# Kernel tuning notes

Measured on AMD Instinct MI355X. Metric: run time of the kernel, lower is better.

Reference implementation:

```python
import jax, jax.numpy as jnp
import numpy as np

N, E, G = 50000, 200000, 2000        # nodes, directed edges, graphs in batch
F_IN, HID, HEADS = 64, 128, 4
DM = HID * HEADS                      # 512, concat GAT output dim
EPS = 1e-5
NEG_SLOPE = 0.2                       # PyG GATConv LeakyReLU slope


def setup_inputs() -> dict:
    key = jax.random.key(0)
    ks = jax.random.split(key, 40)
    rn = lambda k, s, sc: jax.random.normal(k, s, jnp.float32) * sc
    inp = {}
    inp["x"] = rn(ks[0], (N, F_IN), 1.0)
    inp["edge_index"] = jax.random.randint(ks[1], (2, E), 0, N)
    inp["batch"] = jnp.sort(jax.random.randint(ks[2], (N,), 0, G))
    dims = [F_IN, DM, DM]
    for l in range(3):
        d = dims[l]
        inp["W%d" % l] = rn(ks[3 + 4 * l], (d, DM), 1.0 / np.sqrt(d))
        inp["as%d" % l] = rn(ks[4 + 4 * l], (HEADS, HID), 0.1)
        inp["ad%d" % l] = rn(ks[5 + 4 * l], (HEADS, HID), 0.1)
        inp["b%d" % l] = jnp.zeros((DM,), jnp.float32)
        inp["g%d" % l] = jnp.ones((DM,), jnp.float32)
        inp["be%d" % l] = jnp.zeros((DM,), jnp.float32)
    inp["c1w"] = rn(ks[20], (2 * DM, HID), 1.0 / np.sqrt(2 * DM))
    inp["c1b"] = jnp.zeros((HID,), jnp.float32)
    inp["c2w"] = rn(ks[21], (HID, HID // 2), 1.0 / np.sqrt(HID))
    inp["c2b"] = jnp.zeros((HID // 2,), jnp.float32)
    inp["c3w"] = rn(ks[22], (HID // 2, 1), 1.0 / np.sqrt(HID // 2))
    inp["c3b"] = jnp.zeros((1,), jnp.float32)
    return inp


def _gat(x, src, dst, W, a_s, a_d, b):
    """PyG GATConv (heads=HEADS, concat) with self-loops already in src/dst."""
    n = x.shape[0]
    h = (x @ W).reshape(n, HEADS, HID)                     # [N,H,D]
    s_src = jnp.sum(h * a_s, -1)                           # [N,H]
    s_dst = jnp.sum(h * a_d, -1)                           # [N,H]
    e = jax.nn.leaky_relu(s_src[src] + s_dst[dst], NEG_SLOPE)  # [Et,H]
    # segment softmax over incoming edges of each dst node (stable)
    m = jax.lax.stop_gradient(jax.ops.segment_max(e, dst, num_segments=n))
    ex = jnp.exp(e - m[dst])
    alpha = ex / jax.ops.segment_sum(ex, dst, num_segments=n)[dst]
    out = jax.ops.segment_sum(h[src] * alpha[:, :, None], dst, num_segments=n)
    return out.reshape(n, HEADS * HID) + b


def _bn(x, g, b):
    mu = jnp.mean(x, 0)
    var = jnp.var(x, 0)
    return (x - mu) * jax.lax.rsqrt(var + EPS) * g + b


def _forward(x, edge_index, batch, layers, c1w, c1b, c2w, c2b, c3w, c3b):
    loops = jnp.arange(N)
    src = jnp.concatenate([edge_index[0], loops])          # add self-loops
    dst = jnp.concatenate([edge_index[1], loops])
    for (W, a_s, a_d, b, g, be) in layers:
        x = jax.nn.relu(_bn(_gat(x, src, dst, W, a_s, a_d, b), g, be))
    cnt = jax.ops.segment_sum(jnp.ones((N,), x.dtype), batch, num_segments=G)
    mean = jax.ops.segment_sum(x, batch, num_segments=G) / jnp.maximum(cnt, 1.0)[:, None]
    mx = jax.ops.segment_max(x, batch, num_segments=G)
    mx = jnp.where(cnt[:, None] > 0, mx, 0.0)
    h = jnp.concatenate([mean, mx], 1)                     # [G, 2*DM]
    h = jax.nn.relu(h @ c1w + c1b)
    h = jax.nn.relu(h @ c2w + c2b)
    return jax.nn.sigmoid(h @ c3w + c3b).squeeze(-1)       # [G]


def reference(x, edge_index, batch, W0, as0, ad0, b0, g0, be0, W1, as1, ad1, b1, g1, be1, W2, as2, ad2, b2, g2, be2, c1w, c1b, c2w, c2b, c3w, c3b):
    layers = [(W0, as0, ad0, b0, g0, be0), (W1, as1, ad1, b1, g1, be1), (W2, as2, ad2, b2, g2, be2)]
    return _forward(x, edge_index, batch, layers, c1w, c1b, c2w, c2b, c3w, c3b)
```

## Files before the change

### kernel.cpp

```cpp
#include <hip/hip_runtime.h>

#define N_NODES 50000
#define E_EDGES 200000
#define ET_EDGES (E_EDGES + N_NODES)
#define G_GRAPHS 2000
#define F_IN 64
#define HID 128
#define HEADS 4
#define DM 512
#define BN_EPS 1e-5f
#define NEG_SLOPE 0.2f
#define YBLK 391
#define NCHUNK (YBLK / 8)

typedef unsigned short ushort_t;
typedef float floatx4 __attribute__((ext_vector_type(4)));
typedef short short8 __attribute__((ext_vector_type(8)));

__device__ __forceinline__ float b2f(unsigned int u) {
    union { unsigned int i; float f; } v; v.i = u << 16; return v.f;
}
__device__ __forceinline__ ushort_t f2b(float f) {
    union { float f; unsigned int i; } v; v.f = f;
    unsigned int r = v.i + 0x7FFFu + ((v.i >> 16) & 1u);
    return (ushort_t)(r >> 16);
}
__device__ __forceinline__ void unpack8(uint4 v, float* f) {
    f[0] = b2f(v.x & 0xffffu); f[1] = b2f(v.x >> 16);
    f[2] = b2f(v.y & 0xffffu); f[3] = b2f(v.y >> 16);
    f[4] = b2f(v.z & 0xffffu); f[5] = b2f(v.z >> 16);
    f[6] = b2f(v.w & 0xffffu); f[7] = b2f(v.w >> 16);
}
__device__ __forceinline__ void glds16(const ushort_t* g, ushort_t* l) {
    __builtin_amdgcn_global_load_lds(
        (const __attribute__((address_space(1))) unsigned int*)g,
        (__attribute__((address_space(3))) unsigned int*)l, 16, 0, 0);
}

#define XN (N_NODES * F_IN)
#define W0N (F_IN * DM)
#define W1N (DM * DM)
__global__ __launch_bounds__(256) void k_prep(const float* __restrict__ x,
                                              const float* __restrict__ w0,
                                              const float* __restrict__ w1,
                                              const float* __restrict__ w2,
                                              ushort_t* __restrict__ Xb,
                                              ushort_t* __restrict__ Wh0,
                                              ushort_t* __restrict__ Wh1,
                                              ushort_t* __restrict__ Wh2) {
    int t = blockIdx.x * 256 + threadIdx.x;
    if (t < XN) { Xb[t] = f2b(x[t]); return; }
    t -= XN;
    if (t < W0N) {
        int k = t >> 9, n = t & 511;
        Wh0[(size_t)n * F_IN + k] = f2b(w0[t]);
        return;
    }
    t -= W0N;
    if (t < W1N) {
        int k = t >> 9, n = t & 511;
        Wh1[(size_t)n * DM + k] = f2b(w1[t]);
        return;
    }
    t -= W1N;
    if (t < W1N) {
        int k = t >> 9, n = t & 511;
        Wh2[(size_t)n * DM + k] = f2b(w2[t]);
    }
}

__global__ __launch_bounds__(256) void k_wsprep(const float* __restrict__ w0,
                                                const float* __restrict__ as0, const float* __restrict__ ad0,
                                                const float* __restrict__ w1,
                                                const float* __restrict__ as1, const float* __restrict__ ad1,
                                                const float* __restrict__ w2,
                                                const float* __restrict__ as2, const float* __restrict__ ad2,
                                                ushort_t* __restrict__ ws0,
                                                ushort_t* __restrict__ ws1,
                                                ushort_t* __restrict__ ws2) {
    int b = blockIdx.x;
    int l = b >> 3, h = (b >> 1) & 3, v = b & 1;
    const float* w = l == 0 ? w0 : l == 1 ? w1 : w2;
    const float* a = v == 0 ? (l == 0 ? as0 : l == 1 ? as1 : as2)
                            : (l == 0 ? ad0 : l == 1 ? ad1 : ad2);
    ushort_t* o = l == 0 ? ws0 : l == 1 ? ws1 : ws2;
    int K = l == 0 ? F_IN : DM;
    __shared__ float av[HID];
    int t = threadIdx.x;
    if (t < HID) av[t] = a[h * HID + t];
    __syncthreads();
    for (int k = t; k < K; k += 256) {
        const float* wr = w + (size_t)k * DM + h * HID;
        float s = 0.f;
#pragma unroll 8
        for (int c = 0; c < HID; ++c) s += wr[c] * av[c];
        o[(h * 2 + v) * K + k] = f2b(s);
    }
}

__global__ __launch_bounds__(256) void k_mgemm(const ushort_t* __restrict__ A,
                                               const ushort_t* __restrict__ Bh,
                                               const ushort_t* __restrict__ ws,
                                               ushort_t* __restrict__ C,
                                               float* __restrict__ ssrc,
                                               float* __restrict__ sdst,
                                               int M, int K) {
    __shared__ __align__(16) ushort_t Ash[2][128 * 32];
    __shared__ __align__(16) ushort_t Bsh[2][128 * 32];
    int bid = blockIdx.x;
    int head, yb;
    if (bid < NCHUNK * 32) {
        int chunk = bid >> 5, pos = bid & 31;
        yb = chunk * 8 + (pos & 7);
        head = pos >> 3;
    } else {
        int rem = bid - NCHUNK * 32;
        head = rem & 3;
        yb = NCHUNK * 8 + (rem >> 2);
    }
    int m0 = yb * 128, n0 = head * 128;
    int tid = threadIdx.x;
    int lane = tid & 63, wave = tid >> 6;
    int wm = (wave >> 1) * 64, wn = (wave & 1) * 64;
    floatx4 acc[4][4] = {};
    floatx4 sacc[4] = {};
    int lrow = lane >> 2, lchunk = lane & 3;
    int fs = (lrow & 3) ^ ((lrow >> 2) & 3);
    int schunk = lchunk ^ fs;
    int ar0 = wave * 16 + lrow;
    int ar1 = ar0 + 64;
    int gr0 = m0 + ar0; if (gr0 >= M) gr0 = M - 1;
    int gr1 = m0 + ar1; if (gr1 >= M) gr1 = M - 1;
    const ushort_t* gA0 = A + (size_t)gr0 * K + schunk * 8;
    const ushort_t* gA1 = A + (size_t)gr1 * K + schunk * 8;
    const ushort_t* gB0 = Bh + (size_t)(n0 + ar0) * K + schunk * 8;
    const ushort_t* gB1 = Bh + (size_t)(n0 + ar1) * K + schunk * 8;
    int rF = lane & 15, q = lane >> 4;
    int swz = ((q ^ (rF & 3) ^ ((rF >> 2) & 3))) * 8;
    const ushort_t* wsp = ws + (size_t)(head * 2 + (rF & 1)) * K + q * 8;
    auto STAGE = [&](int b, int koff) {
        glds16(gA0 + koff, &Ash[b][(wave * 16) * 32]);
        glds16(gA1 + koff, &Ash[b][(wave * 16 + 64) * 32]);
        glds16(gB0 + koff, &Bsh[b][(wave * 16) * 32]);
        glds16(gB1 + koff, &Bsh[b][(wave * 16 + 64) * 32]);
    };
    STAGE(0, 0);
    __syncthreads();
    int cur = 0;
    for (int k0 = 0; k0 < K; k0 += 32) {
        if (k0 + 32 < K) STAGE(cur ^ 1, k0 + 32);
        short8 sf = *(const short8*)&wsp[k0];
        short8 af[4], bf[4];
#pragma unroll
        for (int i = 0; i < 4; ++i)
            af[i] = *(const short8*)&Ash[cur][(wm + i * 16 + rF) * 32 + swz];
#pragma unroll
        for (int j = 0; j < 4; ++j)
            bf[j] = *(const short8*)&Bsh[cur][(wn + j * 16 + rF) * 32 + swz];
#pragma unroll
        for (int i = 0; i < 4; ++i) {
            sacc[i] = __builtin_amdgcn_mfma_f32_16x16x32_bf16(af[i], sf, sacc[i], 0, 0, 0);
#pragma unroll
            for (int j = 0; j < 4; ++j)
                acc[i][j] = __builtin_amdgcn_mfma_f32_16x16x32_bf16(af[i], bf[j], acc[i][j], 0, 0, 0);
        }
        __syncthreads();
        cur ^= 1;
    }
    int cr = (lane >> 4) * 4, cc = lane & 15;
#pragma unroll
    for (int i = 0; i < 4; ++i) {
#pragma unroll
        for (int r = 0; r < 4; ++r) {
            int gr = m0 + wm + i * 16 + cr + r;
            if (gr < M) {
#pragma unroll
                for (int j = 0; j < 4; ++j)
                    C[(size_t)gr * DM + n0 + wn + j * 16 + cc] = f2b(acc[i][j][r]);
                if (cc == 0) ssrc[gr * 4 + head] = sacc[i][r];
                else if (cc == 1) sdst[gr * 4 + head] = sacc[i][r];
            }
        }
    }
}

__global__ __launch_bounds__(256) void k_bnapply(const ushort_t* __restrict__ X,
                                                 const float* __restrict__ stat,
                                                 const float* __restrict__ gam,
                                                 const float* __restrict__ bet,
                                                 ushort_t* __restrict__ Y) {
    __shared__ float sc[512], sh[512];
    int t = threadIdx.x;
    for (int f = t; f < 512; f += 256) {
        float mu = stat[f] * (1.f / (float)N_NODES);
        float var = fmaxf(stat[512 + f] * (1.f / (float)N_NODES) - mu * mu, 0.f);
        float rs = rsqrtf(var + BN_EPS);
        float s = gam[f] * rs;
        sc[f] = s;
        sh[f] = bet[f] - mu * s;
    }
    __syncthreads();
    int c8 = (t & 63) * 8;
    const float* scp = sc + c8;
    const float* shp = sh + c8;
    for (int n = blockIdx.x * 4 + (t >> 6); n < N_NODES; n += gridDim.x * 4) {
        uint4 v = *(const uint4*)&X[(size_t)n * DM + c8];
        float fv[8]; unpack8(v, fv);
        uint4 ov; unsigned* po = (unsigned*)&ov;
#pragma unroll
        for (int j = 0; j < 4; ++j) {
            unsigned lo = f2b(fmaxf(fv[2 * j] * scp[2 * j] + shp[2 * j], 0.f));
            unsigned hi = f2b(fmaxf(fv[2 * j + 1] * scp[2 * j + 1] + shp[2 * j + 1], 0.f));
            po[j] = lo | (hi << 16);
        }
        *(uint4*)&Y[(size_t)n * DM + c8] = ov;
    }
}

__global__ void k_degree(const int* __restrict__ ei, int* __restrict__ deg) {
    int e = blockIdx.x * blockDim.x + threadIdx.x;
    if (e >= ET_EDGES) return;
    int d = (e < E_EDGES) ? ei[E_EDGES + e] : (e - E_EDGES);
    atomicAdd(&deg[d], 1);
}

__global__ __launch_bounds__(1024) void k_scan3(const int* __restrict__ deg,
                                                int* __restrict__ offs,
                                                int* __restrict__ cursor) {
    __shared__ int wsum[16];
    __shared__ int carry;
    int t = threadIdx.x;
    int lane = t & 63, wv = t >> 6;
    if (t == 0) carry = 0;
    __syncthreads();
    for (int base = 0; base < N_NODES; base += 1024) {
        int i = base + t;
        int v = (i < N_NODES) ? deg[i] : 0;
        int x = v;
#pragma unroll
        for (int off = 1; off < 64; off <<= 1) {
            int y = __shfl_up(x, off);
            if (lane >= off) x += y;
        }
        if (lane == 63) wsum[wv] = x;
        __syncthreads();
        int wpre = 0;
#pragma unroll
        for (int w = 0; w < 16; ++w) wpre += (w < wv) ? wsum[w] : 0;
        int incl = wpre + x;
        if (i < N_NODES) { int o = carry + (incl - v); offs[i] = o; cursor[i] = o; }
        __syncthreads();
        if (t == 1023) carry += incl;
        __syncthreads();
    }
    if (t == 0) offs[N_NODES] = carry;
}

__global__ void k_scatter(const int* __restrict__ ei, int* __restrict__ cursor,
                          int* __restrict__ csr_src) {
    int e = blockIdx.x * blockDim.x + threadIdx.x;
    if (e >= ET_EDGES) return;
    int sv, d;
    if (e < E_EDGES) { sv = ei[e]; d = ei[E_EDGES + e]; } else { sv = d = e - E_EDGES; }
    int pos = atomicAdd(&cursor[d], 1);
    csr_src[pos] = sv;
}

__global__ void k_gbounds(const int* __restrict__ batch, int* __restrict__ gstart) {
    int i = blockIdx.x * blockDim.x + threadIdx.x;
    if (i >= N_NODES) return;
    int b = batch[i];
    int p = (i == 0) ? -1 : batch[i - 1];
    for (int g = p + 1; g <= b; ++g) gstart[g] = i;
    if (i == N_NODES - 1)
        for (int g = b + 1; g <= G_GRAPHS; ++g) gstart[g] = N_NODES;
}

__global__ __launch_bounds__(256) void k_aggregate(const ushort_t* __restrict__ H,
                                                   const float* __restrict__ ssrc,
                                                   const float* __restrict__ sdst,
                                                   const int* __restrict__ offs,
                                                   const int* __restrict__ csr_src,
                                                   const float* __restrict__ bias,
                                                   ushort_t* __restrict__ out) {
    int wave = threadIdx.x >> 6, lane = threadIdx.x & 63;
    int n = blockIdx.x * 4 + wave;
    if (n >= N_NODES) return;
    int beg = offs[n], end = offs[n + 1];
    int hl = lane >> 4, li = lane & 15;
    float sdh = sdst[n * 4 + hl];
    float m = -1e30f, s = 0.f;
    for (int e = beg + li; e < end; e += 16) {
        float sc = ssrc[csr_src[e] * 4 + hl] + sdh;
        sc = sc > 0.f ? sc : NEG_SLOPE * sc;
        if (sc > m) { s = s * __expf(m - sc) + 1.f; m = sc; }
        else s += __expf(sc - m);
    }
#pragma unroll
    for (int mk = 1; mk < 16; mk <<= 1) {
        float om = __shfl_xor(m, mk), os = __shfl_xor(s, mk);
        float mn = fmaxf(m, om);
        s = s * __expf(m - mn) + os * __expf(om - mn);
        m = mn;
    }
    float mh = m, inv = 1.f / s;
    float acc[8] = { 0.f, 0.f, 0.f, 0.f, 0.f, 0.f, 0.f, 0.f };
    int e = beg;
    for (; e + 4 <= end; e += 4) {
        int sv0 = csr_src[e], sv1 = csr_src[e + 1];
        int sv2 = csr_src[e + 2], sv3 = csr_src[e + 3];
        float s0 = ssrc[sv0 * 4 + hl], s1 = ssrc[sv1 * 4 + hl];
        float s2 = ssrc[sv2 * 4 + hl], s3 = ssrc[sv3 * 4 + hl];
        uint4 h0 = *(const uint4*)&H[(size_t)sv0 * DM + lane * 8];
        uint4 h1 = *(const uint4*)&H[(size_t)sv1 * DM + lane * 8];
        uint4 h2 = *(const uint4*)&H[(size_t)sv2 * DM + lane * 8];
        uint4 h3 = *(const uint4*)&H[(size_t)sv3 * DM + lane * 8];
        s0 += sdh; s0 = s0 > 0.f ? s0 : NEG_SLOPE * s0;
        s1 += sdh; s1 = s1 > 0.f ? s1 : NEG_SLOPE * s1;
        s2 += sdh; s2 = s2 > 0.f ? s2 : NEG_SLOPE * s2;
        s3 += sdh; s3 = s3 > 0.f ? s3 : NEG_SLOPE * s3;
        float a0 = __expf(s0 - mh) * inv, a1 = __expf(s1 - mh) * inv;
        float a2 = __expf(s2 - mh) * inv, a3 = __expf(s3 - mh) * inv;
        float f0[8], f1[8], f2[8], f3[8];
        unpack8(h0, f0); unpack8(h1, f1); unpack8(h2, f2); unpack8(h3, f3);
#pragma unroll
        for (int j = 0; j < 8; ++j)
            acc[j] += a0 * f0[j] + a1 * f1[j] + a2 * f2[j] + a3 * f3[j];
    }
    for (; e < end; ++e) {
        int sv = csr_src[e];
        float sc = ssrc[sv * 4 + hl] + sdh;
        sc = sc > 0.f ? sc : NEG_SLOPE * sc;
        float alpha = __expf(sc - mh) * inv;
        uint4 hv = *(const uint4*)&H[(size_t)sv * DM + lane * 8];
        float f[8]; unpack8(hv, f);
#pragma unroll
        for (int j = 0; j < 8; ++j) acc[j] += alpha * f[j];
    }
    const float* bp = bias + lane * 8;
    float4 b0 = *(const float4*)bp;
    float4 b1 = *(const float4*)(bp + 4);
    acc[0] += b0.x; acc[1] += b0.y; acc[2] += b0.z; acc[3] += b0.w;
    acc[4] += b1.x; acc[5] += b1.y; acc[6] += b1.z; acc[7] += b1.w;
    uint4 ov; unsigned* po = (unsigned*)&ov;
#pragma unroll
    for (int j = 0; j < 4; ++j)
        po[j] = (unsigned)f2b(acc[2 * j]) | ((unsigned)f2b(acc[2 * j + 1]) << 16);
    *(uint4*)&out[(size_t)n * DM + lane * 8] = ov;
}

#define BN_ROWS 125
__global__ __launch_bounds__(256) void k_bnstats(const ushort_t* __restrict__ X,
                                                 float* __restrict__ stat) {
    int t = threadIdx.x;
    int c2 = t * 2;
    int beg = blockIdx.x * BN_ROWS;
    int end = beg + BN_ROWS; if (end > N_NODES) end = N_NODES;
    float s0 = 0.f, s1 = 0.f, q0 = 0.f, q1 = 0.f;
    for (int n = beg; n < end; ++n) {
        unsigned v = *(const unsigned*)&X[(size_t)n * DM + c2];
        float x0 = b2f(v & 0xffffu), x1 = b2f(v >> 16);
        s0 += x0; s1 += x1;
        q0 += x0 * x0; q1 += x1 * x1;
    }
    atomicAdd(&stat[c2], s0);
    atomicAdd(&stat[c2 + 1], s1);
    atomicAdd(&stat[512 + c2], q0);
    atomicAdd(&stat[512 + c2 + 1], q1);
}

__global__ __launch_bounds__(64) void k_pool(const ushort_t* __restrict__ X,
                                             const int* __restrict__ gstart,
                                             const float* __restrict__ stat,
                                             const float* __restrict__ gam,
                                             const float* __restrict__ bet,
                                             float* __restrict__ pool) {
    int g = blockIdx.x, t = threadIdx.x;
    int beg = gstart[g], end = gstart[g + 1];
    float sc[8], sh[8];
#pragma unroll
    for (int j = 0; j < 8; ++j) {
        int f = t * 8 + j;
        float mu = stat[f] * (1.f / (float)N_NODES);
        float var = fmaxf(stat[512 + f] * (1.f / (float)N_NODES) - mu * mu, 0.f);
        float rs = rsqrtf(var + BN_EPS);
        sc[j] = gam[f] * rs;
        sh[j] = bet[f] - mu * sc[j];
    }
    float sum[8] = { 0 }, mx[8];
#pragma unroll
    for (int j = 0; j < 8; ++j) mx[j] = -1e30f;
    for (int nn = beg; nn < end; ++nn) {
        uint4 xv = *(const uint4*)&X[(size_t)nn * DM + t * 8];
        float f[8]; unpack8(xv, f);
#pragma unroll
        for (int j = 0; j < 8; ++j) {
            f[j] = fmaxf(f[j] * sc[j] + sh[j], 0.f);
            sum[j] += f[j]; mx[j] = fmaxf(mx[j], f[j]);
        }
    }
    float cnt = (float)(end - beg);
    float inv = cnt > 0.f ? 1.f / cnt : 0.f;
#pragma unroll
    for (int j = 0; j < 8; ++j) {
        pool[(size_t)g * 1024 + t * 8 + j] = sum[j] * inv;
        pool[(size_t)g * 1024 + 512 + t * 8 + j] = cnt > 0.f ? mx[j] : 0.f;
    }
}

__global__ __launch_bounds__(256) void k_mlp(const float* __restrict__ pool,
                                             const float* __restrict__ c1w,
                                             const float* __restrict__ c1b,
                                             const float* __restrict__ c2w,
                                             const float* __restrict__ c2b,
                                             const float* __restrict__ c3w,
                                             const float* __restrict__ c3b,
                                             float* __restrict__ out) {
    __shared__ float row[1024];
    __shared__ float part[128];
    __shared__ float h1[128];
    __shared__ float h2[64];
    int g = blockIdx.x, t = threadIdx.x;
    for (int i = t; i < 1024; i += 256) row[i] = pool[(size_t)g * 1024 + i];
    __syncthreads();
    int half = t >> 7, c = t & 127;
    int k0 = half * 512;
    float a1 = 0.f;
#pragma unroll 8
    for (int k = 0; k < 512; ++k) a1 += row[k0 + k] * c1w[(k0 + k) * 128 + c];
    if (half) part[c] = a1;
    __syncthreads();
    if (!half) h1[c] = fmaxf(a1 + part[c] + c1b[c], 0.f);
    __syncthreads();
    if (t < 64) {
        float a2 = c2b[t];
#pragma unroll 8
        for (int k = 0; k < 128; ++k) a2 += h1[k] * c2w[k * 64 + t];
        h2[t] = fmaxf(a2, 0.f);
    }
    __syncthreads();
    if (t < 64) {
        float p = h2[t] * c3w[t];
#pragma unroll
        for (int off = 32; off > 0; off >>= 1) p += __shfl_down(p, off);
        if (t == 0) {
            float z = p + c3b[0];
            out[g] = 1.f / (1.f + __expf(-z));
        }
    }
}

extern "C" void kernel_launch(void* const* d_in, const int* in_sizes, int n_in,
                              void* d_out, int out_size, void* d_ws, size_t ws_size,
                              hipStream_t stream) {
    const float* x = (const float*)d_in[0];
    const int* ei = (const int*)d_in[1];
    const int* batch = (const int*)d_in[2];
    const float* c1w = (const float*)d_in[21];
    const float* c1b = (const float*)d_in[22];
    const float* c2w = (const float*)d_in[23];
    const float* c2b = (const float*)d_in[24];
    const float* c3w = (const float*)d_in[25];
    const float* c3b = (const float*)d_in[26];

    char* p = (char*)d_ws;
    auto carve = [&](size_t bytes) -> char* {
        char* r = p; p += (bytes + 255) & ~(size_t)255; return r;
    };
    ushort_t* buf0   = (ushort_t*)carve((size_t)N_NODES * DM * 2);
    ushort_t* buf1   = (ushort_t*)carve((size_t)N_NODES * DM * 2);
    ushort_t* Xb     = (ushort_t*)carve((size_t)N_NODES * F_IN * 2);
    ushort_t* Wh0    = (ushort_t*)carve((size_t)F_IN * DM * 2);
    ushort_t* Wh1    = (ushort_t*)carve((size_t)DM * DM * 2);
    ushort_t* Wh2    = (ushort_t*)carve((size_t)DM * DM * 2);
    ushort_t* ws0    = (ushort_t*)carve((size_t)8 * F_IN * 2);
    ushort_t* ws1    = (ushort_t*)carve((size_t)8 * DM * 2);
    ushort_t* ws2    = (ushort_t*)carve((size_t)8 * DM * 2);
    float*    ssrc   = (float*)carve((size_t)N_NODES * 4 * 4);
    float*    sdst   = (float*)carve((size_t)N_NODES * 4 * 4);
    int*      deg    = (int*)carve((size_t)N_NODES * 4);
    int*      offs   = (int*)carve((size_t)(N_NODES + 1) * 4);
    int*      cursor = (int*)carve((size_t)N_NODES * 4);
    int*      csrsrc = (int*)carve((size_t)ET_EDGES * 4);
    float*    bnstat = (float*)carve(3 * 1024 * 4);
    int*      gstart = (int*)carve((size_t)(G_GRAPHS + 1) * 4);
    float*    pool   = (float*)carve((size_t)G_GRAPHS * 1024 * 4);

    hipMemsetAsync(deg, 0, (size_t)N_NODES * 4, stream);
    hipMemsetAsync(bnstat, 0, 3 * 1024 * 4, stream);
    k_degree<<<(ET_EDGES + 255) / 256, 256, 0, stream>>>(ei, deg);
    k_scan3<<<1, 1024, 0, stream>>>(deg, offs, cursor);
    k_scatter<<<(ET_EDGES + 255) / 256, 256, 0, stream>>>(ei, cursor, csrsrc);
    k_gbounds<<<(N_NODES + 255) / 256, 256, 0, stream>>>(batch, gstart);
    {
        int total = XN + W0N + 2 * W1N;
        k_prep<<<(total + 255) / 256, 256, 0, stream>>>(
            x, (const float*)d_in[3], (const float*)d_in[9], (const float*)d_in[15],
            Xb, Wh0, Wh1, Wh2);
    }
    k_wsprep<<<24, 256, 0, stream>>>(
        (const float*)d_in[3], (const float*)d_in[4], (const float*)d_in[5],
        (const float*)d_in[9], (const float*)d_in[10], (const float*)d_in[11],
        (const float*)d_in[15], (const float*)d_in[16], (const float*)d_in[17],
        ws0, ws1, ws2);

    const ushort_t* Whs[3] = { Wh0, Wh1, Wh2 };
    const ushort_t* wss[3] = { ws0, ws1, ws2 };
    const float* pgam = nullptr;
    const float* pbet = nullptr;
    const ushort_t* in = Xb;
    for (int l = 0; l < 3; ++l) {
        int K = (l == 0) ? F_IN : DM;
        const float* bia = (const float*)d_in[6 + 6 * l];
        const float* gam = (const float*)d_in[7 + 6 * l];
        const float* bet = (const float*)d_in[8 + 6 * l];
        ushort_t* h   = (l % 2 == 0) ? buf1 : buf0;
        ushort_t* agg = (l % 2 == 0) ? buf0 : buf1;

        k_mgemm<<<4 * YBLK, 256, 0, stream>>>(
            in, Whs[l], wss[l], h, ssrc, sdst, N_NODES, K);
        k_aggregate<<<(N_NODES + 3) / 4, 256, 0, stream>>>(h, ssrc, sdst, offs, csrsrc, bia, agg);
        k_bnstats<<<(N_NODES + BN_ROWS - 1) / BN_ROWS, 256, 0, stream>>>(agg, bnstat + l * 1024);
        if (l < 2)
            k_bnapply<<<2048, 256, 0, stream>>>(agg, bnstat + l * 1024, gam, bet, h);
        in = h;
        pgam = gam; pbet = bet;
    }
    k_pool<<<G_GRAPHS, 64, 0, stream>>>(buf0, gstart, bnstat + 2 * 1024, pgam, pbet, pool);
    k_mlp<<<G_GRAPHS, 256, 0, stream>>>(pool, c1w, c1b, c2w, c2b, c3w, c3b,
                                        (float*)d_out);
}
```

Before: 705.3 us.

## Triple-buffer GEMM tiles with vmcnt waits and stage score weights in LDS

The projection GEMM moves from a double-buffered loop with two full __syncthreads per iteration to a three-stage ring. Prefetch now runs two k-steps ahead, and each step waits only on its own tile with s_waitcnt vmcnt(4) plus a single raw s_barrier. The attention-score weight vectors are also loaded into LDS once per block instead of being read from global memory on every k-step. The aim is to hide global-load latency and cut synchronisation. The cost is more LDS per block, which may lower occupancy, and correctness now depends on the hand-written vmcnt counts matching the four async loads per stage.

```diff
diff --git a/kernel.cpp b/kernel.cpp
--- a/kernel.cpp
+++ b/kernel.cpp
@@ -105,8 +105,9 @@
                                                float* __restrict__ ssrc,
                                                float* __restrict__ sdst,
                                                int M, int K) {
-    __shared__ __align__(16) ushort_t Ash[2][128 * 32];
-    __shared__ __align__(16) ushort_t Bsh[2][128 * 32];
+    __shared__ __align__(16) ushort_t Ash[3][128 * 32];
+    __shared__ __align__(16) ushort_t Bsh[3][128 * 32];
+    __shared__ __align__(16) ushort_t wsh[2 * 512];
     int bid = blockIdx.x;
     int head, yb;
     if (bid < NCHUNK * 32) {
@@ -124,6 +125,8 @@
     int wm = (wave >> 1) * 64, wn = (wave & 1) * 64;
     floatx4 acc[4][4] = {};
     floatx4 sacc[4] = {};
+    for (int i = tid; i < 2 * K; i += 256)
+        wsh[i] = ws[(size_t)head * 2 * K + i];
     int lrow = lane >> 2, lchunk = lane & 3;
     int fs = (lrow & 3) ^ ((lrow >> 2) & 3);
     int schunk = lchunk ^ fs;
@@ -137,26 +140,31 @@
     const ushort_t* gB1 = Bh + (size_t)(n0 + ar1) * K + schunk * 8;
     int rF = lane & 15, q = lane >> 4;
     int swz = ((q ^ (rF & 3) ^ ((rF >> 2) & 3))) * 8;
-    const ushort_t* wsp = ws + (size_t)(head * 2 + (rF & 1)) * K + q * 8;
-    auto STAGE = [&](int b, int koff) {
-        glds16(gA0 + koff, &Ash[b][(wave * 16) * 32]);
-        glds16(gA1 + koff, &Ash[b][(wave * 16 + 64) * 32]);
-        glds16(gB0 + koff, &Bsh[b][(wave * 16) * 32]);
-        glds16(gB1 + koff, &Bsh[b][(wave * 16 + 64) * 32]);
+    ushort_t* As0 = &Ash[0][0]; ushort_t* As1 = &Ash[1][0]; ushort_t* As2 = &Ash[2][0];
+    ushort_t* Bs0 = &Bsh[0][0]; ushort_t* Bs1 = &Bsh[1][0]; ushort_t* Bs2 = &Bsh[2][0];
+    auto STAGE = [&](ushort_t* Ab, ushort_t* Bb, int koff) {
+        glds16(gA0 + koff, Ab + (wave * 16) * 32);
+        glds16(gA1 + koff, Ab + (wave * 16 + 64) * 32);
+        glds16(gB0 + koff, Bb + (wave * 16) * 32);
+        glds16(gB1 + koff, Bb + (wave * 16 + 64) * 32);
     };
-    STAGE(0, 0);
-    __syncthreads();
-    int cur = 0;
+    __syncthreads();
+    STAGE(As0, Bs0, 0);
+    if (K > 32) STAGE(As1, Bs1, 32);
     for (int k0 = 0; k0 < K; k0 += 32) {
-        if (k0 + 32 < K) STAGE(cur ^ 1, k0 + 32);
-        short8 sf = *(const short8*)&wsp[k0];
+        if (k0 + 32 < K) asm volatile("s_waitcnt vmcnt(4)" ::: "memory");
+        else             asm volatile("s_waitcnt vmcnt(0)" ::: "memory");
+        __builtin_amdgcn_s_barrier();
+        __builtin_amdgcn_sched_barrier(0);
+        if (k0 + 64 < K) STAGE(As2, Bs2, k0 + 64);
+        short8 sf = *(const short8*)&wsh[(rF & 1) * K + q * 8 + k0];
         short8 af[4], bf[4];
 #pragma unroll
         for (int i = 0; i < 4; ++i)
-            af[i] = *(const short8*)&Ash[cur][(wm + i * 16 + rF) * 32 + swz];
+            af[i] = *(const short8*)&As0[(wm + i * 16 + rF) * 32 + swz];
 #pragma unroll
         for (int j = 0; j < 4; ++j)
-            bf[j] = *(const short8*)&Bsh[cur][(wn + j * 16 + rF) * 32 + swz];
+            bf[j] = *(const short8*)&Bs0[(wn + j * 16 + rF) * 32 + swz];
 #pragma unroll
         for (int i = 0; i < 4; ++i) {
             sacc[i] = __builtin_amdgcn_mfma_f32_16x16x32_bf16(af[i], sf, sacc[i], 0, 0, 0);
@@ -164,8 +172,8 @@
             for (int j = 0; j < 4; ++j)
                 acc[i][j] = __builtin_amdgcn_mfma_f32_16x16x32_bf16(af[i], bf[j], acc[i][j], 0, 0, 0);
         }
-        __syncthreads();
-        cur ^= 1;
+        ushort_t* tA = As0; As0 = As1; As1 = As2; As2 = tA;
+        ushort_t* tB = Bs0; Bs0 = Bs1; Bs1 = Bs2; Bs2 = tB;
     }
     int cr = (lane >> 4) * 4, cc = lane & 15;
 #pragma unroll
```

New measurement: 707.9 us. No clear change (+0.4%).
